# Performance work log

Hardware: AMD Instinct MI355X
Metric: run time of the kernel (lower is better)

Reference implementation:

```python
import jax, jax.numpy as jnp
import numpy as np

EMB = 512
H1, H2 = 300, 100


def setup_inputs() -> dict:
    key = jax.random.key(0)
    ks = jax.random.split(key, 12)
    B, N, M = 2, 256, 256
    inp = {
        "action_embedding": jax.random.normal(ks[0], (B, EMB, N), jnp.float32),
        "anchor_embedding": jax.random.normal(ks[1], (B, EMB, M), jnp.float32),
        "action_points": jax.random.normal(ks[2], (B, 3, N), jnp.float32),
        "anchor_points": jax.random.normal(ks[3], (B, 3, M), jnp.float32),
        # MLPKernel params: Linear(1024,300), Linear(300,100), Linear(100,1), stored as [in,out]
        "W1": jax.random.normal(ks[4], (2 * EMB, H1), jnp.float32) / np.sqrt(2 * EMB),
        "b1": jax.random.normal(ks[5], (H1,), jnp.float32) * 0.01,
        "W2": jax.random.normal(ks[6], (H1, H2), jnp.float32) / np.sqrt(H1),
        "b2": jax.random.normal(ks[7], (H2,), jnp.float32) * 0.01,
        "W3": jax.random.normal(ks[8], (H2, 1), jnp.float32) / np.sqrt(H2),
        "b3": jax.random.normal(ks[9], (1,), jnp.float32) * 0.01,
    }
    return inp


def _pairwise_radii(Phi_A, Phi_B, W1, b1, W2, b2, W3, b3):
    # MLPKernel: softplus((mlp(cat(a,b)) + mlp(cat(b,a))) / 2) over all (n, m) pairs.
    # Split first linear: cat(x1,x2) @ W1 == x1 @ Wa + x2 @ Wb  (no [B,N,M,1024] materialization).
    F = Phi_A.shape[-1]
    Wa, Wb = W1[:F], W1[F:]
    hA_a = jnp.einsum('bnf,fh->bnh', Phi_A, Wa)
    hA_b = jnp.einsum('bnf,fh->bnh', Phi_A, Wb)
    hB_a = jnp.einsum('bmf,fh->bmh', Phi_B, Wa)
    hB_b = jnp.einsum('bmf,fh->bmh', Phi_B, Wb)

    def mlp_rest(h):  # h: [B,N,M,H1] pre-bias first-layer activations
        h = jax.nn.relu(h + b1)
        h = jax.nn.relu(jnp.einsum('bnmh,hk->bnmk', h, W2) + b2)
        return jnp.einsum('bnmk,ko->bnmo', h, W3) + b3

    v1 = mlp_rest(hA_a[:, :, None, :] + hB_b[:, None, :, :])  # mlp(cat(A_n, B_m))
    v2 = mlp_rest(hB_a[:, None, :, :] + hA_b[:, :, None, :])  # mlp(cat(B_m, A_n))
    return jax.nn.softplus((v1 + v2) * 0.5)[..., 0]  # [B,N,M]


def _multilaterate(P, R, W):
    # Vectorized estimate_p over batch b and query point n.
    # P: [B,M,3] anchor points, R: [B,N,M] estimated radii, W: [B,M] weights.
    M = P.shape[1]
    norm2 = jnp.sum(P * P, axis=-1)                      # [B,M]  (Pt @ P)
    d = norm2[:, None, :] - R ** 2                       # [B,N,M]  PtP - r^2
    a = jnp.einsum('bm,bnm,bmd->bnd', W, d, P) / M       # [B,N,3]
    WPPt = jnp.einsum('bm,bmd,bme->bde', W, P, P) / M    # [B,3,3]  mean(W * P Pt)
    mWd = jnp.einsum('bm,bnm->bn', W, d) / M             # [B,N]    mean(W * (PtP - r^2))
    c = jnp.einsum('bm,bmd->bd', W, P) / M               # [B,3]
    # B @ c with B = -2*mean(W*PPt) - mean(W*d)*I
    Bc = -2.0 * jnp.einsum('bde,be->bd', WPPt, c)[:, None, :] - mWd[..., None] * c[:, None, :]
    cc = jnp.sum(c * c, axis=-1)                         # [B]
    f = a + Bc + 2.0 * cc[:, None, None] * c[:, None, :]  # [B,N,3]
    PPt_mean = jnp.einsum('bmd,bme->bde', P, P) / M       # unweighted mean(PPt)
    H = -2.0 * PPt_mean + 2.0 * jnp.einsum('bd,be->bde', c, c)  # [B,3,3]
    Hinv = jnp.linalg.inv(H)
    q = -jnp.einsum('bde,bne->bnd', Hinv, f)
    return q + c[:, None, :]                              # [B,N,3]


def reference(action_embedding, anchor_embedding, action_points, anchor_points,
              W1, b1, W2, b2, W3, b3):
    P_A = jnp.transpose(action_points, (0, 2, 1))    # [B,N,3]
    P_B = jnp.transpose(anchor_points, (0, 2, 1))    # [B,M,3]
    Phi_A = jnp.transpose(action_embedding, (0, 2, 1))  # [B,N,F]
    Phi_B = jnp.transpose(anchor_embedding, (0, 2, 1))  # [B,M,F]
    B_weights = jnp.ones(Phi_B.shape[:2], dtype=Phi_B.dtype)
    R_est = _pairwise_radii(Phi_A, Phi_B, W1, b1, W2, b2, W3, b3)
    P_A_B_pred = _multilaterate(P_B, R_est, B_weights)  # [B,N,3]
    flow = jnp.transpose(P_A_B_pred - P_A, (0, 2, 1))   # [B,3,N] == full_flow (pred_weight=False)
    return flow
```

## Files before the change

kernel.cpp:

```cpp
#include <hip/hip_runtime.h>
#include <hip/hip_bf16.h>
#include <math.h>

#define EMB 512
#define H1 300
#define H2 100
#define NB 2
#define NN 256
#define MM 256

#define OFF_HAA 0
#define OFF_HAB 153600
#define OFF_HBA 307200
#define OFF_HBB 460800
#define OFF_S   614400
#define OFF_CST 616448
#define OFF_W2C 616512
#define OFF_B2P 634432
#define OFF_W3P 634544
#define OFF_ET  634656
#define OFF_W1T 896800
#define OFF_V   1060640

typedef __attribute__((ext_vector_type(8))) short bf16x8;
typedef __attribute__((ext_vector_type(4))) float f32x4;

static __device__ inline unsigned f2bfbits(float f) {
    union { float f; unsigned u; } v; v.f = f;
    return (v.u + 0x7fffu + ((v.u >> 16) & 1u)) >> 16;
}
static __device__ inline unsigned pack_bf2(float a, float b) {
    union { __hip_bfloat162 h; unsigned u; } cv;
    cv.h = __float22bfloat162_rn(make_float2(a, b));
    return cv.u;
}

__global__ __launch_bounds__(256) void k_setup(
    const float* __restrict__ W1, const float* __restrict__ W2,
    const float* __restrict__ b2, const float* __restrict__ W3,
    const float* __restrict__ actE, const float* __restrict__ ancE,
    const float* __restrict__ ancP, float* __restrict__ ws)
{
    __shared__ float Tf[32 * 36];
    __shared__ float red[4][13];
    int blk = blockIdx.x;
    int tid = threadIdx.x;

    if (blk < 320) {
        unsigned short* W1t = (unsigned short*)(ws + OFF_W1T);
        int h0 = (blk % 20) * 32, f0 = (blk / 20) * 32;
        int fr = tid >> 3, hc4 = (tid & 7) * 4;
        int hg = h0 + hc4;
        float4 v = make_float4(0.f, 0.f, 0.f, 0.f);
        if (hg < 600) {
            int half = (hg >= 300) ? 1 : 0;
            int hh = hg - half * 300;
            v = *(const float4*)&W1[(size_t)(half * EMB + f0 + fr) * H1 + hh];
        }
        *(float4*)&Tf[fr * 36 + hc4] = v;
        __syncthreads();
        int hr = tid >> 3, f4 = (tid & 7) * 4;
        float v0 = Tf[(f4 + 0) * 36 + hr];
        float v1 = Tf[(f4 + 1) * 36 + hr];
        float v2 = Tf[(f4 + 2) * 36 + hr];
        float v3 = Tf[(f4 + 3) * 36 + hr];
        uint2 pk = make_uint2(pack_bf2(v0, v1), pack_bf2(v2, v3));
        *(uint2*)&W1t[(size_t)(h0 + hr) * EMB + f0 + f4] = pk;
    } else if (blk < 832) {
        int i = blk - 320;
        unsigned short* Et = (unsigned short*)(ws + OFF_ET);
        int f0 = (i & 15) * 32;
        int n0 = ((i >> 4) & 7) * 32;
        int bs = i >> 7, b = bs >> 1, src = bs & 1;
        const float* E = (src == 0 ? actE : ancE) + (size_t)b * EMB * NN;
        int r = tid >> 3, c4 = (tid & 7) * 4;
        float4 v = *(const float4*)&E[(size_t)(f0 + r) * NN + n0 + c4];
        *(float4*)&Tf[r * 36 + c4] = v;
        __syncthreads();
        int nr = tid >> 3, f4 = (tid & 7) * 4;
        float v0 = Tf[(f4 + 0) * 36 + nr];
        float v1 = Tf[(f4 + 1) * 36 + nr];
        float v2 = Tf[(f4 + 2) * 36 + nr];
        float v3 = Tf[(f4 + 3) * 36 + nr];
        uint2 pk = make_uint2(pack_bf2(v0, v1), pack_bf2(v2, v3));
        *(uint2*)&Et[((size_t)(bs * NN) + n0 + nr) * EMB + f0 + f4] = pk;
    } else if (blk < 848) {
        int i = blk - 832;
        unsigned short* W2c = (unsigned short*)(ws + OFF_W2C);
        int start = i * 256 + tid;
        for (int idx = start; idx < 10*112*32; idx += 16 * 256) {
            int c  = idx / 3584;
            int r  = idx - c * 3584;
            int j  = r >> 5;
            int kk = r & 31;
            int k  = c * 32 + kk;
            float v = (j < H2 && k < H1) ? W2[k * H2 + j] : 0.0f;
            W2c[idx] = (unsigned short)f2bfbits(v);
        }
        if (i == 0 && tid < 112) {
            int j = tid;
            ws[OFF_B2P + j] = (j < H2) ? b2[j] : 0.0f;
            ws[OFF_W3P + j] = (j < H2) ? W3[j] : 0.0f;
        }
    } else {
        int b = blk - 848;
        float* cst = ws + OFF_CST;
        int m = tid;
        float px = ancP[b*3*MM + 0*MM + m];
        float py = ancP[b*3*MM + 1*MM + m];
        float pz = ancP[b*3*MM + 2*MM + m];
        float n2 = px*px + py*py + pz*pz;

        float v[13];
        v[0]=px; v[1]=py; v[2]=pz;
        v[3]=px*px; v[4]=px*py; v[5]=px*pz; v[6]=py*py; v[7]=py*pz; v[8]=pz*pz;
        v[9]=n2*px; v[10]=n2*py; v[11]=n2*pz; v[12]=n2;

        #pragma unroll
        for (int off = 32; off >= 1; off >>= 1) {
            #pragma unroll
            for (int q = 0; q < 13; q++) v[q] += __shfl_xor(v[q], off, 64);
        }
        int wave = tid >> 6, lane = tid & 63;
        if (lane == 0) {
            #pragma unroll
            for (int q = 0; q < 13; q++) red[wave][q] = v[q];
        }
        __syncthreads();
        if (tid == 0) {
            float s[13];
            #pragma unroll
            for (int q = 0; q < 13; q++)
                s[q] = red[0][q] + red[1][q] + red[2][q] + red[3][q];
            const float invM = 1.0f / MM;
            float c0 = s[0]*invM, c1 = s[1]*invM, c2 = s[2]*invM;
            float Pxx = s[3]*invM, Pxy = s[4]*invM, Pxz = s[5]*invM;
            float Pyy = s[6]*invM, Pyz = s[7]*invM, Pzz = s[8]*invM;

            float H00 = -2.0f*Pxx + 2.0f*c0*c0;
            float H01 = -2.0f*Pxy + 2.0f*c0*c1;
            float H02 = -2.0f*Pxz + 2.0f*c0*c2;
            float H11 = -2.0f*Pyy + 2.0f*c1*c1;
            float H12 = -2.0f*Pyz + 2.0f*c1*c2;
            float H22 = -2.0f*Pzz + 2.0f*c2*c2;
            float H10 = H01, H20 = H02, H21 = H12;

            float det = H00*(H11*H22 - H12*H21)
                      - H01*(H10*H22 - H12*H20)
                      + H02*(H10*H21 - H11*H20);
            float id = 1.0f / det;
            float i00 = (H11*H22 - H12*H21)*id;
            float i01 = (H02*H21 - H01*H22)*id;
            float i02 = (H01*H12 - H02*H11)*id;
            float i10 = (H12*H20 - H10*H22)*id;
            float i11 = (H00*H22 - H02*H20)*id;
            float i12 = (H02*H10 - H00*H12)*id;
            float i20 = (H10*H21 - H11*H20)*id;
            float i21 = (H01*H20 - H00*H21)*id;
            float i22 = (H00*H11 - H01*H10)*id;

            float t0x = -2.0f*(Pxx*c0 + Pxy*c1 + Pxz*c2);
            float t0y = -2.0f*(Pxy*c0 + Pyy*c1 + Pyz*c2);
            float t0z = -2.0f*(Pxz*c0 + Pyz*c1 + Pzz*c2);
            float cc = c0*c0 + c1*c1 + c2*c2;

            float* C = cst + b*32;
            C[0]=c0; C[1]=c1; C[2]=c2;
            C[3]=i00; C[4]=i01; C[5]=i02;
            C[6]=i10; C[7]=i11; C[8]=i12;
            C[9]=i20; C[10]=i21; C[11]=i22;
            C[12]=t0x; C[13]=t0y; C[14]=t0z;
            C[15]=cc;
            C[16]=s[9]*invM; C[17]=s[10]*invM; C[18]=s[11]*invM; C[19]=s[12]*invM;
        }
    }
}

__global__ __launch_bounds__(256) void k_hidden(
    float* __restrict__ ws, const float* __restrict__ b1)
{
    int bs = blockIdx.z, b = bs >> 1, src = bs & 1;
    int n0 = blockIdx.x * 16;
    int h0 = blockIdx.y * 64;
    const unsigned short* Et  = (const unsigned short*)(ws + OFF_ET)
                                + (size_t)(bs * NN) * EMB;
    const unsigned short* W1t = (const unsigned short*)(ws + OFF_W1T);
    float* outA = ws + (src == 0 ? OFF_HAA : OFF_HBA) + (size_t)b * NN * H1;
    float* outB = ws + (src == 0 ? OFF_HAB : OFF_HBB) + (size_t)b * NN * H1;

    __shared__ unsigned short EtL[16 * 40];
    __shared__ unsigned short W1tL[64 * 40];

    int tid = threadIdx.x;
    int lane = tid & 63, w = tid >> 6;
    int colj = lane & 15, quad = lane >> 4;

    int er  = tid >> 4, ek2 = (tid & 15) * 2;
    int wr  = tid >> 2, wk8 = (tid & 3) * 8;

    f32x4 acc = (f32x4){0.f, 0.f, 0.f, 0.f};

    for (int c = 0; c < 16; c++) {
        int k0 = c * 32;
        unsigned ev = *(const unsigned*)&Et[(size_t)(n0 + er) * EMB + k0 + ek2];
        uint4 wv = *(const uint4*)&W1t[(size_t)(h0 + wr) * EMB + k0 + wk8];
        __syncthreads();
        *(unsigned*)&EtL[er * 40 + ek2] = ev;
        *(uint4*)&W1tL[wr * 40 + wk8] = wv;
        __syncthreads();
        bf16x8 af = *(const bf16x8*)&EtL[colj * 40 + quad * 8];
        bf16x8 bf = *(const bf16x8*)&W1tL[(w * 16 + colj) * 40 + quad * 8];
        acc = __builtin_amdgcn_mfma_f32_16x16x32_bf16(af, bf, acc, 0, 0, 0);
    }

    int hg = h0 + w * 16 + colj;
    if (hg < 600) {
        int hh = (hg < 300) ? hg : hg - 300;
        float* o = (hg < 300) ? outA : outB;
        float bias = (src == 0) ? b1[hh] : 0.0f;
        #pragma unroll
        for (int r = 0; r < 4; r++) {
            int n = n0 + quad * 4 + r;
            o[(size_t)n * H1 + hh] = acc[r] + bias;
        }
    }
}

__global__ __launch_bounds__(256) void k_pair(
    const float* __restrict__ ws_f, const float* __restrict__ b3p,
    float* __restrict__ V)
{
    int bz = blockIdx.z, b = bz >> 1, p = bz & 1;
    int n0 = blockIdx.y * 16, m0 = blockIdx.x * 16;
    int tid = threadIdx.x;
    int lane = tid & 63, w = tid >> 6;
    int colj = lane & 15, quad = lane >> 4;

    __shared__ float hAfL[16 * 36];
    __shared__ float hBfL[16 * 36];
    __shared__ short W2L[112 * 40];

    const unsigned short* W2c = (const unsigned short*)(ws_f + OFF_W2C);
    float b2v[7], w3v[7];
    #pragma unroll
    for (int jt = 0; jt < 7; jt++) {
        b2v[jt] = ws_f[OFF_B2P + jt * 16 + colj];
        w3v[jt] = ws_f[OFF_W3P + jt * 16 + colj];
    }
    float b3val = b3p[0];

    const float* srcX = ws_f + (p == 0 ? OFF_HAA : OFF_HAB) + (size_t)(b*NN + n0) * H1;
    const float* srcY = ws_f + (p == 0 ? OFF_HBB : OFF_HBA) + (size_t)(b*NN + m0) * H1;

    int sarr = tid >> 7;
    int srow = (tid >> 3) & 15;
    int sseg = tid & 7;
    const float* ssrc = (sarr ? srcY : srcX) + srow * H1;
    float* sdst = (sarr ? hBfL : hAfL) + srow * 36 + sseg * 4;

    f32x4 acc[4][7];
    #pragma unroll
    for (int i = 0; i < 4; i++)
        #pragma unroll
        for (int jt = 0; jt < 7; jt++)
            acc[i][jt] = (f32x4){0.f,0.f,0.f,0.f};

    for (int c = 0; c < 10; c++) {
        float4 sv = *(const float4*)&ssrc[c * 32 + sseg * 4];
        const uint4* wsrc4 = (const uint4*)W2c + c * 448;
        uint4 w0 = wsrc4[tid];
        uint4 w1 = wsrc4[(tid + 256) % 448];

        __syncthreads();
        *(float4*)sdst = sv;
        {
            int j = tid >> 2, q = tid & 3;
            *(uint4*)&W2L[j * 40 + q * 8] = w0;
            if (tid < 192) {
                int u2 = tid + 256;
                *(uint4*)&W2L[(u2 >> 2) * 40 + (u2 & 3) * 8] = w1;
            }
        }
        __syncthreads();

        float4 hb0 = *(const float4*)&hBfL[colj * 36 + quad * 8];
        float4 hb1 = *(const float4*)&hBfL[colj * 36 + quad * 8 + 4];
        bf16x8 bfr[7];
        #pragma unroll
        for (int jt = 0; jt < 7; jt++)
            bfr[jt] = *(const bf16x8*)&W2L[(jt * 16 + colj) * 40 + quad * 8];

        #pragma unroll
        for (int i = 0; i < 4; i++) {
            const float* xa = &hAfL[(w * 4 + i) * 36 + quad * 8];
            float4 ha0 = *(const float4*)&xa[0];
            float4 ha1 = *(const float4*)&xa[4];
            union { unsigned u[4]; bf16x8 v; } af;
            af.u[0] = pack_bf2(fmaxf(ha0.x + hb0.x, 0.f), fmaxf(ha0.y + hb0.y, 0.f));
            af.u[1] = pack_bf2(fmaxf(ha0.z + hb0.z, 0.f), fmaxf(ha0.w + hb0.w, 0.f));
            af.u[2] = pack_bf2(fmaxf(ha1.x + hb1.x, 0.f), fmaxf(ha1.y + hb1.y, 0.f));
            af.u[3] = pack_bf2(fmaxf(ha1.z + hb1.z, 0.f), fmaxf(ha1.w + hb1.w, 0.f));
            #pragma unroll
            for (int jt = 0; jt < 7; jt++)
                acc[i][jt] = __builtin_amdgcn_mfma_f32_16x16x32_bf16(
                    af.v, bfr[jt], acc[i][jt], 0, 0, 0);
        }
    }

    float vsum[4][4];
    #pragma unroll
    for (int i = 0; i < 4; i++)
        #pragma unroll
        for (int r = 0; r < 4; r++) vsum[i][r] = 0.0f;
    #pragma unroll
    for (int i = 0; i < 4; i++)
        #pragma unroll
        for (int jt = 0; jt < 7; jt++)
            #pragma unroll
            for (int r = 0; r < 4; r++)
                vsum[i][r] = fmaf(fmaxf(acc[i][jt][r] + b2v[jt], 0.f),
                                  w3v[jt], vsum[i][r]);

    #pragma unroll
    for (int i = 0; i < 4; i++)
        #pragma unroll
        for (int r = 0; r < 4; r++) {
            float v = vsum[i][r];
            v += __shfl_xor(v, 1, 16);
            v += __shfl_xor(v, 2, 16);
            v += __shfl_xor(v, 4, 16);
            v += __shfl_xor(v, 8, 16);
            vsum[i][r] = v;
        }

    if (colj == 0) {
        #pragma unroll
        for (int i = 0; i < 4; i++) {
            int n = n0 + w * 4 + i;
            float4 o;
            o.x = 0.5f * (vsum[i][0] + b3val);
            o.y = 0.5f * (vsum[i][1] + b3val);
            o.z = 0.5f * (vsum[i][2] + b3val);
            o.w = 0.5f * (vsum[i][3] + b3val);
            *(float4*)&V[(((size_t)p * NB + b) * NN + n) * MM + m0 + quad * 4] = o;
        }
    }
}

__global__ void k_finish(const float* __restrict__ V, const float* __restrict__ ancP,
                         const float* __restrict__ cst, const float* __restrict__ actP,
                         float* __restrict__ out)
{
    int b = blockIdx.y;
    int n = blockIdx.x * 16 + (threadIdx.x >> 4);
    int ml = threadIdx.x & 15;
    const float* v0 = V + (((size_t)0 * NB + b) * NN + n) * MM;
    const float* v1 = V + (((size_t)1 * NB + b) * NN + n) * MM;
    float s0 = 0.f, s1 = 0.f, s2 = 0.f, s3 = 0.f;
    #pragma unroll
    for (int k = 0; k < 16; k++) {
        int m = ml + k * 16;
        float x = v0[m] + v1[m];
        float R = fmaxf(x, 0.f) + log1pf(expf(-fabsf(x)));
        float r2 = R * R;
        float px = ancP[b*3*MM + 0*MM + m];
        float py = ancP[b*3*MM + 1*MM + m];
        float pz = ancP[b*3*MM + 2*MM + m];
        s0 = fmaf(r2, px, s0);
        s1 = fmaf(r2, py, s1);
        s2 = fmaf(r2, pz, s2);
        s3 += r2;
    }
    #pragma unroll
    for (int off = 8; off >= 1; off >>= 1) {
        s0 += __shfl_xor(s0, off, 16);
        s1 += __shfl_xor(s1, off, 16);
        s2 += __shfl_xor(s2, off, 16);
        s3 += __shfl_xor(s3, off, 16);
    }
    if (ml == 0) {
        const float* C = cst + b*32;
        float c0=C[0], c1=C[1], c2=C[2];
        float t0x=C[12], t0y=C[13], t0z=C[14];
        float cc=C[15];
        float SnP0=C[16], SnP1=C[17], SnP2=C[18], Sn=C[19];

        const float invM = 1.0f / MM;
        float a0 = SnP0 - s0*invM;
        float a1 = SnP1 - s1*invM;
        float a2 = SnP2 - s2*invM;
        float mWd = Sn - s3*invM;

        float f0 = a0 + t0x - mWd*c0 + 2.0f*cc*c0;
        float f1 = a1 + t0y - mWd*c1 + 2.0f*cc*c1;
        float f2 = a2 + t0z - mWd*c2 + 2.0f*cc*c2;

        float q0 = -(C[3]*f0 + C[4]*f1 + C[5]*f2);
        float q1 = -(C[6]*f0 + C[7]*f1 + C[8]*f2);
        float q2 = -(C[9]*f0 + C[10]*f1 + C[11]*f2);

        float p0 = q0 + c0, p1 = q1 + c1, p2 = q2 + c2;

        out[b*3*NN + 0*NN + n] = p0 - actP[b*3*NN + 0*NN + n];
        out[b*3*NN + 1*NN + n] = p1 - actP[b*3*NN + 1*NN + n];
        out[b*3*NN + 2*NN + n] = p2 - actP[b*3*NN + 2*NN + n];
    }
}

extern "C" void kernel_launch(void* const* d_in, const int* in_sizes, int n_in,
                              void* d_out, int out_size, void* d_ws, size_t ws_size,
                              hipStream_t stream)
{
    const float* actE = (const float*)d_in[0];
    const float* ancE = (const float*)d_in[1];
    const float* actP = (const float*)d_in[2];
    const float* ancP = (const float*)d_in[3];
    const float* W1   = (const float*)d_in[4];
    const float* b1   = (const float*)d_in[5];
    const float* W2   = (const float*)d_in[6];
    const float* b2   = (const float*)d_in[7];
    const float* W3   = (const float*)d_in[8];
    const float* b3   = (const float*)d_in[9];
    float* ws  = (float*)d_ws;
    float* out = (float*)d_out;

    k_setup <<<850, 256, 0, stream>>>(W1, W2, b2, W3, actE, ancE, ancP, ws);
    k_hidden<<<dim3(16, 10, 4), 256, 0, stream>>>(ws, b1);
    k_pair  <<<dim3(16, 16, NB*2), 256, 0, stream>>>(ws, b3, ws + OFF_V);
    k_finish<<<dim3(16, NB), 256, 0, stream>>>(ws + OFF_V, ancP, ws + OFF_CST, actP, out);
}
```

Before: 126.4 us.

## Stage full hidden rows in LDS once and read W2 fragments directly from global

The pair kernel now loads the whole 16x300 hA and hB tiles into shared memory in one pass before the loop, padding the tail columns with zeros. This replaces the per-chunk staging that needed two barriers in each of ten iterations. W2 bf16 fragments are read straight from global memory (L1/L2 cached) instead of being copied to LDS, and the chunk loop is fully unrolled. Launch bounds now request two blocks per SM, which trades barrier and LDS-copy overhead for larger LDS use and more global-load latency exposed inside the MFMA loop.

```diff
diff --git a/kernel.cpp b/kernel.cpp
--- a/kernel.cpp
+++ b/kernel.cpp
@@ -13,7 +13,6 @@
 #define OFF_HAB 153600
 #define OFF_HBA 307200
 #define OFF_HBB 460800
-#define OFF_S   614400
 #define OFF_CST 616448
 #define OFF_W2C 616512
 #define OFF_B2P 634432
@@ -226,7 +225,9 @@
     }
 }
 
-__global__ __launch_bounds__(256) void k_pair(
+#define SH 308
+
+__global__ __launch_bounds__(256, 2) void k_pair(
     const float* __restrict__ ws_f, const float* __restrict__ b3p,
     float* __restrict__ V)
 {
@@ -236,9 +237,8 @@
     int lane = tid & 63, w = tid >> 6;
     int colj = lane & 15, quad = lane >> 4;
 
-    __shared__ float hAfL[16 * 36];
-    __shared__ float hBfL[16 * 36];
-    __shared__ short W2L[112 * 40];
+    __shared__ float hAf[16 * SH];
+    __shared__ float hBf[16 * SH];
 
     const unsigned short* W2c = (const unsigned short*)(ws_f + OFF_W2C);
     float b2v[7], w3v[7];
@@ -252,11 +252,22 @@
     const float* srcX = ws_f + (p == 0 ? OFF_HAA : OFF_HAB) + (size_t)(b*NN + n0) * H1;
     const float* srcY = ws_f + (p == 0 ? OFF_HBB : OFF_HBA) + (size_t)(b*NN + m0) * H1;
 
-    int sarr = tid >> 7;
-    int srow = (tid >> 3) & 15;
-    int sseg = tid & 7;
-    const float* ssrc = (sarr ? srcY : srcX) + srow * H1;
-    float* sdst = (sarr ? hBfL : hAfL) + srow * 36 + sseg * 4;
+    for (int idx = tid; idx < 2464; idx += 256) {
+        int a = (idx >= 1232) ? 1 : 0;
+        int k = idx - a * 1232;
+        int row, c4;
+        float4 v = make_float4(0.f, 0.f, 0.f, 0.f);
+        if (k < 1200) {
+            row = k / 75; c4 = k - row * 75;
+            v = *(const float4*)&(a ? srcY : srcX)[row * H1 + c4 * 4];
+        } else {
+            int j = k - 1200;
+            row = j >> 1; c4 = 75 + (j & 1);
+        }
+        float* dst = (a ? hBf : hAf) + row * SH + c4 * 4;
+        *(float4*)dst = v;
+    }
+    __syncthreads();
 
     f32x4 acc[4][7];
     #pragma unroll
@@ -265,34 +276,19 @@
         for (int jt = 0; jt < 7; jt++)
             acc[i][jt] = (f32x4){0.f,0.f,0.f,0.f};
 
+    #pragma unroll
     for (int c = 0; c < 10; c++) {
-        float4 sv = *(const float4*)&ssrc[c * 32 + sseg * 4];
-        const uint4* wsrc4 = (const uint4*)W2c + c * 448;
-        uint4 w0 = wsrc4[tid];
-        uint4 w1 = wsrc4[(tid + 256) % 448];
-
-        __syncthreads();
-        *(float4*)sdst = sv;
-        {
-            int j = tid >> 2, q = tid & 3;
-            *(uint4*)&W2L[j * 40 + q * 8] = w0;
-            if (tid < 192) {
-                int u2 = tid + 256;
-                *(uint4*)&W2L[(u2 >> 2) * 40 + (u2 & 3) * 8] = w1;
-            }
-        }
-        __syncthreads();
-
-        float4 hb0 = *(const float4*)&hBfL[colj * 36 + quad * 8];
-        float4 hb1 = *(const float4*)&hBfL[colj * 36 + quad * 8 + 4];
         bf16x8 bfr[7];
         #pragma unroll
         for (int jt = 0; jt < 7; jt++)
-            bfr[jt] = *(const bf16x8*)&W2L[(jt * 16 + colj) * 40 + quad * 8];
+            bfr[jt] = *(const bf16x8*)&W2c[c * 3584 + (jt * 16 + colj) * 32 + quad * 8];
+
+        float4 hb0 = *(const float4*)&hBf[colj * SH + c * 32 + quad * 8];
+        float4 hb1 = *(const float4*)&hBf[colj * SH + c * 32 + quad * 8 + 4];
 
         #pragma unroll
         for (int i = 0; i < 4; i++) {
-            const float* xa = &hAfL[(w * 4 + i) * 36 + quad * 8];
+            const float* xa = &hAf[(w * 4 + i) * SH + c * 32 + quad * 8];
             float4 ha0 = *(const float4*)&xa[0];
             float4 ha1 = *(const float4*)&xa[4];
             union { unsigned u[4]; bf16x8 v; } af;
```

Result: no change. 125.5 us (median of 2 runs) (-0.7%).
